# Optimization experiments

Measured on AMD Instinct MI355X. Metric: run time of the kernel, lower is better.

## Reference

```python
import jax, jax.numpy as jnp
import numpy as np

NUM_QUBITS = 10
NUM_LAYERS = 5
OBS = 10          # observation_size == num_qubits (required by input_scaling indexing)
NUM_OUTPUTS = 4   # num_actions, discretize=False
BATCH = 4096


def _bcast(theta, n):
    # theta: scalar or (B,) -> broadcastable against (B, 2, 2, ..., 2)
    return jnp.reshape(jnp.asarray(theta), (-1,) + (1,) * n)


def _ry(st, theta, q, n):
    # st: (B,) + (2,)*n complex64; per-sample RY(theta) on qubit q
    t = _bcast(theta, n) * 0.5
    c, s = jnp.cos(t), jnp.sin(t)
    s0 = jax.lax.index_in_dim(st, 0, axis=q + 1, keepdims=True)
    s1 = jax.lax.index_in_dim(st, 1, axis=q + 1, keepdims=True)
    return jnp.concatenate([c * s0 - s * s1, s * s0 + c * s1], axis=q + 1)


def _rz(st, theta, q, n):
    t = _bcast(theta, n) * 0.5
    s0 = jax.lax.index_in_dim(st, 0, axis=q + 1, keepdims=True)
    s1 = jax.lax.index_in_dim(st, 1, axis=q + 1, keepdims=True)
    return jnp.concatenate([jnp.exp(-1j * t) * s0, jnp.exp(1j * t) * s1], axis=q + 1)


def _cnot(st, c, t):
    # flip target axis on the control=1 slab; pure index ops (no residuals in bwd)
    s0 = jax.lax.index_in_dim(st, 0, axis=c + 1, keepdims=True)
    s1 = jax.lax.index_in_dim(st, 1, axis=c + 1, keepdims=True)
    s1 = jnp.flip(s1, axis=t + 1)
    return jnp.concatenate([s0, s1], axis=c + 1)


def _layer(st, x, isc, w, n, obs):
    # isc: (2n,) input_scaling row, w: (2n,) weights row
    for i in range(obs):
        st = _ry(st, isc[i] * x[:, i], i, n)
        st = _rz(st, isc[i + obs] * x[:, i], i, n)
    for i in range(n):
        st = _rz(st, w[i], i, n)
    for i in range(n):
        st = _ry(st, w[i + n], i, n)
    if n == 2:
        st = _cnot(st, 0, 1)
    else:
        for i in range(n):
            st = _cnot(st, i, (i + 1) % n)
    return st


_layer_ckpt = jax.checkpoint(_layer, static_argnums=(4, 5))


def _circuit(x, input_scaling, weights, n, num_layers, obs, num_outputs):
    B = x.shape[0]
    st = jnp.zeros((B,) + (2,) * n, dtype=jnp.complex64)
    st = st.at[(slice(None),) + (0,) * n].set(1.0)  # |0...0>
    for layer in range(num_layers):
        st = _layer_ckpt(st, x, input_scaling[layer], weights[layer], n, obs)
    probs = jnp.real(st * jnp.conj(st))
    outs = []
    for i in range(num_outputs):
        axes = tuple(a for a in range(1, n + 1) if a != i + 1)
        pi = jnp.sum(probs, axis=axes)  # (B, 2)
        outs.append(pi[:, 0] - pi[:, 1])  # <Z_i>
    return jnp.stack(outs, axis=1)


def setup_inputs() -> dict:
    key = jax.random.key(0)
    k1, k2 = jax.random.split(key)
    x = jax.random.normal(k1, (BATCH, OBS), dtype=jnp.float32)
    input_scaling = jnp.ones((NUM_LAYERS, 2 * NUM_QUBITS), dtype=jnp.float32)
    weights = jax.random.uniform(k2, (NUM_LAYERS, 2 * NUM_QUBITS), minval=-np.pi, maxval=np.pi, dtype=jnp.float32)
    output_scaling = jnp.ones((NUM_OUTPUTS,), dtype=jnp.float32)
    return {"x": x, "input_scaling": input_scaling, "weights": weights, "output_scaling": output_scaling}


def reference(x, input_scaling, weights, output_scaling):
    z = _circuit(x, input_scaling, weights, NUM_QUBITS, NUM_LAYERS, OBS, NUM_OUTPUTS)
    return z * output_scaling  # (B, num_actions); discretize=False -> actions = scaled expvals
```

## Files before the change

kernel.cpp:

```cpp
#include <hip/hip_runtime.h>


constexpr int NQ  = 10;
constexpr int NL  = 5;
constexpr int OBS = 10;

typedef float        f2 __attribute__((ext_vector_type(2)));
typedef _Float16     h2 __attribute__((ext_vector_type(2)));
typedef unsigned int u2 __attribute__((ext_vector_type(2)));
typedef int          i4 __attribute__((ext_vector_type(4)));

__device__ __forceinline__ float readlane_f(float v, int l) {
    return __int_as_float(__builtin_amdgcn_readlane(__float_as_int(v), l));
}
__device__ __forceinline__ int h2_to_i(h2 v) { int i; __builtin_memcpy(&i, &v, 4); return i; }
__device__ __forceinline__ h2  i_to_h2(int i) { h2 v; __builtin_memcpy(&v, &i, 4); return v; }

__device__ __forceinline__ h2 bperm_h2(int byte_addr, h2 v) {
    return i_to_h2(__builtin_amdgcn_ds_bpermute(byte_addr, h2_to_i(v)));
}
template <int CTRL>
__device__ __forceinline__ h2 dpp_h2(h2 v) {
    return i_to_h2(__builtin_amdgcn_update_dpp(0, h2_to_i(v), CTRL, 0xF, 0xF, true));
}
template <int M>
__device__ __forceinline__ h2 swz_h2(h2 v) {
    return i_to_h2(__builtin_amdgcn_ds_swizzle(h2_to_i(v), (M << 10) | 0x1F));
}

#if __has_builtin(__builtin_amdgcn_permlane16_swap) && __has_builtin(__builtin_amdgcn_permlane32_swap)
#define HAVE_PERMLANE_SWAP 1
#else
#define HAVE_PERMLANE_SWAP 0
#endif

__device__ __forceinline__ h2 xor_lane(h2 v, int M, int a16, int a32) {
    switch (M) {
    case 1:  return swz_h2<1>(v);
    case 2:  return swz_h2<2>(v);
    case 4:  return swz_h2<4>(v);
    case 8:  return swz_h2<8>(v);
    case 16: return bperm_h2(a16, v);
    default: return bperm_h2(a32, v);
    }
}

__device__ __forceinline__ float fold16_f(float z, int a16) {
#if HAVE_PERMLANE_SWAP
    u2 r = __builtin_amdgcn_permlane16_swap(
        __float_as_uint(z), __float_as_uint(z), false, false);
    return __uint_as_float(r[0]) + __uint_as_float(r[1]);
#else
    return z + __int_as_float(__builtin_amdgcn_ds_bpermute(a16, __float_as_int(z)));
#endif
}
__device__ __forceinline__ float fold32_f(float z, int a32) {
#if HAVE_PERMLANE_SWAP
    u2 r = __builtin_amdgcn_permlane32_swap(
        __float_as_uint(z), __float_as_uint(z), false, false);
    return __uint_as_float(r[0]) + __uint_as_float(r[1]);
#else
    return z + __int_as_float(__builtin_amdgcn_ds_bpermute(a32, __float_as_int(z)));
#endif
}

__device__ __forceinline__ h2 mk_h2(float a, float b) {
    h2 r; r.x = (_Float16)a; r.y = (_Float16)b; return r;
}
__device__ __forceinline__ h2 xor_h2(h2 v, int m) {
    return i_to_h2(h2_to_i(v) ^ m);
}

__global__ __launch_bounds__(256, 4) void qsim_kernel(
    const float* __restrict__ x,
    const float* __restrict__ isc,
    const float* __restrict__ w,
    const float* __restrict__ oscale,
    float* __restrict__ out,
    int B)
{
    const int lane  = threadIdx.x & 63;
    const int wslot = threadIdx.x >> 6;
    const int wid   = (blockIdx.x * blockDim.x + threadIdx.x) >> 6;
    if (wid >= B) return;

    __shared__ int ldsK[4][50 * 4];

    float cUR, cUI, cVR, cVI;
    {
        const int g   = (lane < 50) ? lane : 49;
        const int q   = g % 10;
        const int lyr = g / 10;
        const float xq    = x[wid * OBS + q];
        const float alpha = isc[lyr * 2 * NQ + q]      * xq;
        const float beta  = isc[lyr * 2 * NQ + NQ + q] * xq;
        const float gamma = w[lyr * 2 * NQ + q];
        const float delta = w[lyr * 2 * NQ + NQ + q];
        float sa, ca, sp, cp, sd, cd;
        __sincosf(0.5f * alpha,          &sa, &ca);
        __sincosf(0.5f * (beta + gamma), &sp, &cp);
        __sincosf(0.5f * delta,          &sd, &cd);
        const float A = cd * ca, Bt = sd * sa;
        const float C = cd * sa, D  = sd * ca;
        cUR = (A - Bt) * cp;
        cUI = -(A + Bt) * sp;
        cVR = (C + D) * cp;
        cVI = (C - D) * sp;
        if (lane < 50) {
            i4 pk;
            pk.x = h2_to_i(mk_h2(cUR,  cUR));
            pk.y = h2_to_i(mk_h2(-cUI, cUI));
            pk.z = h2_to_i(mk_h2(cVR,  cVR));
            pk.w = h2_to_i(mk_h2(-cVI, cVI));
            *reinterpret_cast<i4*>(&ldsK[wslot][lane * 4]) = pk;
        }
    }

    const int a16 = (lane ^ 16) * 4;
    const int a32 = (lane ^ 32) * 4;
    const int cnot_src  = (lane ^ (lane >> 1));
    const int addr_even = cnot_src * 4;
    const int addr_odd  = (cnot_src ^ 32) * 4;

    int smP[6];
#pragma unroll
    for (int qq = 0; qq < 6; ++qq) {
        const int M = 1 << (5 - qq);
        smP[qq] = (lane & M) ? (int)0x80008000 : 0;
    }

    h2 c[16];

    {
        float Lr = 1.f, Li = 0.f;
#pragma unroll
        for (int q = 4; q < 10; ++q) {
            const float ur = readlane_f(cUR, q), ui = readlane_f(cUI, q);
            const float vr = readlane_f(cVR, q), vi = readlane_f(cVI, q);
            const int M = 1 << (9 - q);
            const float fr = (lane & M) ? vr : ur;
            const float fi = (lane & M) ? vi : ui;
            const float nr = Lr * fr - Li * fi;
            const float ni = Lr * fi + Li * fr;
            Lr = nr; Li = ni;
        }
        f2 cf[16];
        cf[0] = (f2){Lr, Li};
#pragma unroll
        for (int r = 1; r < 16; ++r) cf[r] = (f2){0.f, 0.f};
#pragma unroll
        for (int q = 3; q >= 0; --q) {
            const int m = 1 << (3 - q);
            const float ur = readlane_f(cUR, q), ui = readlane_f(cUI, q);
            const float vr = readlane_f(cVR, q), vi = readlane_f(cVI, q);
#pragma unroll
            for (int r0 = 0; r0 < 16; ++r0) {
                if (r0 >= m) continue;
                const f2 s = cf[r0];
                cf[r0 | m] = (f2){ s.x*vr - s.y*vi, s.x*vi + s.y*vr };
                cf[r0]     = (f2){ s.x*ur - s.y*ui, s.x*ui + s.y*ur };
            }
        }
#pragma unroll
        for (int r = 0; r < 16; ++r) c[r] = mk_h2(cf[r].x, cf[r].y);
    }

#define SWAPR(i, j) { h2 _t = c[i]; c[i] = c[j]; c[j] = _t; }

    for (int layer = 0; layer < NL; ++layer) {
        const int base = layer * NQ;

        if (layer > 0) {
            h2 K[NQ][4];
#pragma unroll
            for (int q = 0; q < NQ; ++q) {
                const i4 pk = *reinterpret_cast<const i4*>(
                    &ldsK[wslot][(base + q) * 4]);
                K[q][0] = i_to_h2(pk.x);
                K[q][1] = i_to_h2(pk.y);
                K[q][2] = i_to_h2(pk.z);
                K[q][3] = i_to_h2(pk.w);
            }
#pragma unroll
            for (int q = 0; q < NQ; ++q) {
                const h2 kUU = K[q][0];
                const h2 kUI = K[q][1];
                const h2 kVV = K[q][2];
                const h2 kVI = K[q][3];

                if (q < 4) {
                    const int m = 1 << (3 - q);
#pragma unroll
                    for (int r0 = 0; r0 < 16; ++r0) {
                        if (r0 & m) continue;
                        const int r1 = r0 | m;
                        const h2 c0 = c[r0], c1 = c[r1];
                        const h2 c0s = c0.yx, c1s = c1.yx;
                        c[r0] = kUU*c0 + kUI*c0s - kVV*c1 + kVI*c1s;
                        c[r1] = kVV*c0 + kVI*c0s + kUU*c1 - kUI*c1s;
                    }
                } else {
                    const int  M  = 1 << (9 - q);
                    const int  sm = smP[q - 4];
                    const h2 kPI = xor_h2(kUI, sm);
                    const h2 kQR = xor_h2(-kVV, sm);
#pragma unroll
                    for (int r = 0; r < 16; ++r) {
                        const h2 mv = c[r];
                        const h2 pv = xor_lane(mv, M, a16, a32);
                        c[r] = kUU*mv + kPI*mv.yx + kQR*pv + kVI*pv.yx;
                    }
                }
            }
        }

        if (layer < NL - 1) {
            SWAPR(8, 12) SWAPR(9, 13) SWAPR(10, 14) SWAPR(11, 15)
            SWAPR(4, 6)  SWAPR(5, 7)  SWAPR(12, 14) SWAPR(13, 15)
            SWAPR(2, 3)  SWAPR(6, 7)  SWAPR(10, 11) SWAPR(14, 15)
#pragma unroll
            for (int r = 0; r < 16; ++r) {
                const int addr = (r & 1) ? addr_odd : addr_even;
                c[r] = bperm_h2(addr, c[r]);
            }
            const bool ctl = (lane & 1) != 0;
#pragma unroll
            for (int r = 0; r < 8; ++r) {
                const h2 t0 = c[r], t1 = c[r + 8];
                c[r]     = ctl ? t1 : t0;
                c[r + 8] = ctl ? t0 : t1;
            }
        }
    }

    f2 Z01 = (f2){0.f, 0.f}, Z23 = (f2){0.f, 0.f};
#pragma unroll
    for (int r = 0; r < 16; ++r) {
#if __has_builtin(__builtin_amdgcn_fdot2)
        const float pv = __builtin_amdgcn_fdot2(c[r], c[r], 0.0f, false);
#else
        const float cr = (float)c[r].x, ci = (float)c[r].y;
        const float pv = cr * cr + ci * ci;
#endif
        Z01 += (f2){ (__popc(r & 7)  & 1) ? -pv : pv,
                     (__popc(r & 12) & 1) ? -pv : pv };
        Z23 += (f2){ (__popc(r & 14) & 1) ? -pv : pv,
                     (__popc(r & 15) & 1) ? -pv : pv };
    }
    const float sL = (__popc(lane) & 1) ? -1.f : 1.f;
    float z0 = Z01.x * sL, z1 = Z01.y, z2 = Z23.x, z3 = Z23.y;
#pragma unroll
    for (int m = 1; m < 64; m <<= 1) {
        if (m == 1)      { z0 += __int_as_float(__builtin_amdgcn_update_dpp(0, __float_as_int(z0), 0xB1, 0xF, 0xF, true));
                           z1 += __int_as_float(__builtin_amdgcn_update_dpp(0, __float_as_int(z1), 0xB1, 0xF, 0xF, true));
                           z2 += __int_as_float(__builtin_amdgcn_update_dpp(0, __float_as_int(z2), 0xB1, 0xF, 0xF, true));
                           z3 += __int_as_float(__builtin_amdgcn_update_dpp(0, __float_as_int(z3), 0xB1, 0xF, 0xF, true)); }
        else if (m == 2) { z0 += __int_as_float(__builtin_amdgcn_update_dpp(0, __float_as_int(z0), 0x4E, 0xF, 0xF, true));
                           z1 += __int_as_float(__builtin_amdgcn_update_dpp(0, __float_as_int(z1), 0x4E, 0xF, 0xF, true));
                           z2 += __int_as_float(__builtin_amdgcn_update_dpp(0, __float_as_int(z2), 0x4E, 0xF, 0xF, true));
                           z3 += __int_as_float(__builtin_amdgcn_update_dpp(0, __float_as_int(z3), 0x4E, 0xF, 0xF, true)); }
        else if (m == 4) { z0 += __int_as_float(__builtin_amdgcn_update_dpp(0, __builtin_amdgcn_update_dpp(0, __float_as_int(z0), 0x1B, 0xF, 0xF, true), 0x141, 0xF, 0xF, true));
                           z1 += __int_as_float(__builtin_amdgcn_update_dpp(0, __builtin_amdgcn_update_dpp(0, __float_as_int(z1), 0x1B, 0xF, 0xF, true), 0x141, 0xF, 0xF, true));
                           z2 += __int_as_float(__builtin_amdgcn_update_dpp(0, __builtin_amdgcn_update_dpp(0, __float_as_int(z2), 0x1B, 0xF, 0xF, true), 0x141, 0xF, 0xF, true));
                           z3 += __int_as_float(__builtin_amdgcn_update_dpp(0, __builtin_amdgcn_update_dpp(0, __float_as_int(z3), 0x1B, 0xF, 0xF, true), 0x141, 0xF, 0xF, true)); }
        else if (m == 8) { z0 += __int_as_float(__builtin_amdgcn_update_dpp(0, __float_as_int(z0), 0x128, 0xF, 0xF, true));
                           z1 += __int_as_float(__builtin_amdgcn_update_dpp(0, __float_as_int(z1), 0x128, 0xF, 0xF, true));
                           z2 += __int_as_float(__builtin_amdgcn_update_dpp(0, __float_as_int(z2), 0x128, 0xF, 0xF, true));
                           z3 += __int_as_float(__builtin_amdgcn_update_dpp(0, __float_as_int(z3), 0x128, 0xF, 0xF, true)); }
        else if (m == 16){ z0 = fold16_f(z0, a16);
                           z1 = fold16_f(z1, a16);
                           z2 = fold16_f(z2, a16);
                           z3 = fold16_f(z3, a16); }
        else             { z0 = fold32_f(z0, a32);
                           z1 = fold32_f(z1, a32);
                           z2 = fold32_f(z2, a32);
                           z3 = fold32_f(z3, a32); }
    }
    if (lane == 0) {
        out[wid * 4 + 0] = z0 * oscale[0];
        out[wid * 4 + 1] = z1 * oscale[1];
        out[wid * 4 + 2] = z2 * oscale[2];
        out[wid * 4 + 3] = z3 * oscale[3];
    }
#undef SWAPR
}

extern "C" void kernel_launch(void* const* d_in, const int* in_sizes, int n_in,
                              void* d_out, int out_size, void* d_ws, size_t ws_size,
                              hipStream_t stream) {
    const float* x      = (const float*)d_in[0];
    const float* isc    = (const float*)d_in[1];
    const float* w      = (const float*)d_in[2];
    const float* oscale = (const float*)d_in[3];
    float* out = (float*)d_out;

    const int B = in_sizes[0] / OBS;
    const int threads = 256;
    const int blocks = (B * 64 + threads - 1) / threads;
    qsim_kernel<<<blocks, threads, 0, stream>>>(x, isc, w, oscale, out, B);
}
```

Before: 84.68 us.

## Reorder CNOT select before lane permute and prefetch next layer coefficients

The CNOT ring now does the control-conditioned register select before the cross-lane bpermute, using a precomputed parity predicate, and loads the next layer's LDS coefficients between them so the LDS latency overlaps the permutes. The xor-16 lane exchange switches from bpermute to ds_swizzle. The initial state build uses packed f2 complex multiplies, and the f16 conversion uses cvt_pkrtz. These target LDS and permute latency and the conversion instruction count, in exchange for more live registers from the hoisted coefficient array and round-toward-zero instead of round-to-nearest f16 conversion.

```diff
diff --git a/kernel.cpp b/kernel.cpp
--- a/kernel.cpp
+++ b/kernel.cpp
@@ -19,10 +19,6 @@
 __device__ __forceinline__ h2 bperm_h2(int byte_addr, h2 v) {
     return i_to_h2(__builtin_amdgcn_ds_bpermute(byte_addr, h2_to_i(v)));
 }
-template <int CTRL>
-__device__ __forceinline__ h2 dpp_h2(h2 v) {
-    return i_to_h2(__builtin_amdgcn_update_dpp(0, h2_to_i(v), CTRL, 0xF, 0xF, true));
-}
 template <int M>
 __device__ __forceinline__ h2 swz_h2(h2 v) {
     return i_to_h2(__builtin_amdgcn_ds_swizzle(h2_to_i(v), (M << 10) | 0x1F));
@@ -34,13 +30,13 @@
 #define HAVE_PERMLANE_SWAP 0
 #endif
 
-__device__ __forceinline__ h2 xor_lane(h2 v, int M, int a16, int a32) {
+__device__ __forceinline__ h2 xor_lane(h2 v, int M, int a32) {
     switch (M) {
     case 1:  return swz_h2<1>(v);
     case 2:  return swz_h2<2>(v);
     case 4:  return swz_h2<4>(v);
     case 8:  return swz_h2<8>(v);
-    case 16: return bperm_h2(a16, v);
+    case 16: return swz_h2<16>(v);
     default: return bperm_h2(a32, v);
     }
 }
@@ -66,6 +62,14 @@
 
 __device__ __forceinline__ h2 mk_h2(float a, float b) {
     h2 r; r.x = (_Float16)a; r.y = (_Float16)b; return r;
+}
+__device__ __forceinline__ h2 pk_h2(float a, float b) {
+#if __has_builtin(__builtin_amdgcn_cvt_pkrtz)
+    auto t = __builtin_amdgcn_cvt_pkrtz(a, b);
+    h2 r; __builtin_memcpy(&r, &t, 4); return r;
+#else
+    return mk_h2(a, b);
+#endif
 }
 __device__ __forceinline__ h2 xor_h2(h2 v, int m) {
     return i_to_h2(h2_to_i(v) ^ m);
@@ -121,6 +125,8 @@
     const int cnot_src  = (lane ^ (lane >> 1));
     const int addr_even = cnot_src * 4;
     const int addr_odd  = (cnot_src ^ 32) * 4;
+    const bool ctlE = (__popc(lane) & 1) != 0;
+    const bool ctlO = !ctlE;
 
     int smP[6];
 #pragma unroll
@@ -130,22 +136,34 @@
     }
 
     h2 c[16];
+    h2 Kc[NQ][4];
+
+    auto loadK = [&](int lyr) {
+#pragma unroll
+        for (int q = 0; q < NQ; ++q) {
+            const i4 pk = *reinterpret_cast<const i4*>(
+                &ldsK[wslot][(lyr * NQ + q) * 4]);
+            Kc[q][0] = i_to_h2(pk.x);
+            Kc[q][1] = i_to_h2(pk.y);
+            Kc[q][2] = i_to_h2(pk.z);
+            Kc[q][3] = i_to_h2(pk.w);
+        }
+    };
 
     {
-        float Lr = 1.f, Li = 0.f;
+        f2 L = (f2){1.f, 0.f};
 #pragma unroll
         for (int q = 4; q < 10; ++q) {
             const float ur = readlane_f(cUR, q), ui = readlane_f(cUI, q);
             const float vr = readlane_f(cVR, q), vi = readlane_f(cVI, q);
             const int M = 1 << (9 - q);
-            const float fr = (lane & M) ? vr : ur;
-            const float fi = (lane & M) ? vi : ui;
-            const float nr = Lr * fr - Li * fi;
-            const float ni = Lr * fi + Li * fr;
-            Lr = nr; Li = ni;
+            const bool b = (lane & M) != 0;
+            const f2 F1 = (f2){ b ? vr : ur,  b ? vi : ui };
+            const f2 F2 = (f2){ -F1.y, F1.x };
+            L = (f2){L.x, L.x} * F1 + (f2){L.y, L.y} * F2;
         }
         f2 cf[16];
-        cf[0] = (f2){Lr, Li};
+        cf[0] = L;
 #pragma unroll
         for (int r = 1; r < 16; ++r) cf[r] = (f2){0.f, 0.f};
 #pragma unroll
@@ -153,84 +171,79 @@
             const int m = 1 << (3 - q);
             const float ur = readlane_f(cUR, q), ui = readlane_f(cUI, q);
             const float vr = readlane_f(cVR, q), vi = readlane_f(cVI, q);
+            const f2 U1 = (f2){ur, ui}, U2 = (f2){-ui, ur};
+            const f2 V1 = (f2){vr, vi}, V2 = (f2){-vi, vr};
 #pragma unroll
             for (int r0 = 0; r0 < 16; ++r0) {
                 if (r0 >= m) continue;
-                const f2 s = cf[r0];
-                cf[r0 | m] = (f2){ s.x*vr - s.y*vi, s.x*vi + s.y*vr };
-                cf[r0]     = (f2){ s.x*ur - s.y*ui, s.x*ui + s.y*ur };
+                const f2 s  = cf[r0];
+                const f2 sx = (f2){s.x, s.x}, sy = (f2){s.y, s.y};
+                cf[r0 | m] = sx * V1 + sy * V2;
+                cf[r0]     = sx * U1 + sy * U2;
             }
         }
 #pragma unroll
-        for (int r = 0; r < 16; ++r) c[r] = mk_h2(cf[r].x, cf[r].y);
+        for (int r = 0; r < 16; ++r) c[r] = pk_h2(cf[r].x, cf[r].y);
     }
 
 #define SWAPR(i, j) { h2 _t = c[i]; c[i] = c[j]; c[j] = _t; }
-
-    for (int layer = 0; layer < NL; ++layer) {
-        const int base = layer * NQ;
-
-        if (layer > 0) {
-            h2 K[NQ][4];
-#pragma unroll
-            for (int q = 0; q < NQ; ++q) {
-                const i4 pk = *reinterpret_cast<const i4*>(
-                    &ldsK[wslot][(base + q) * 4]);
-                K[q][0] = i_to_h2(pk.x);
-                K[q][1] = i_to_h2(pk.y);
-                K[q][2] = i_to_h2(pk.z);
-                K[q][3] = i_to_h2(pk.w);
-            }
-#pragma unroll
-            for (int q = 0; q < NQ; ++q) {
-                const h2 kUU = K[q][0];
-                const h2 kUI = K[q][1];
-                const h2 kVV = K[q][2];
-                const h2 kVI = K[q][3];
-
-                if (q < 4) {
-                    const int m = 1 << (3 - q);
-#pragma unroll
-                    for (int r0 = 0; r0 < 16; ++r0) {
-                        if (r0 & m) continue;
-                        const int r1 = r0 | m;
-                        const h2 c0 = c[r0], c1 = c[r1];
-                        const h2 c0s = c0.yx, c1s = c1.yx;
-                        c[r0] = kUU*c0 + kUI*c0s - kVV*c1 + kVI*c1s;
-                        c[r1] = kVV*c0 + kVI*c0s + kUU*c1 - kUI*c1s;
-                    }
-                } else {
-                    const int  M  = 1 << (9 - q);
-                    const int  sm = smP[q - 4];
-                    const h2 kPI = xor_h2(kUI, sm);
-                    const h2 kQR = xor_h2(-kVV, sm);
-#pragma unroll
-                    for (int r = 0; r < 16; ++r) {
-                        const h2 mv = c[r];
-                        const h2 pv = xor_lane(mv, M, a16, a32);
-                        c[r] = kUU*mv + kPI*mv.yx + kQR*pv + kVI*pv.yx;
-                    }
+#define RING(nextL)                                                     \
+    {                                                                   \
+        SWAPR(8, 12) SWAPR(9, 13) SWAPR(10, 14) SWAPR(11, 15)           \
+        SWAPR(4, 6)  SWAPR(5, 7)  SWAPR(12, 14) SWAPR(13, 15)           \
+        SWAPR(2, 3)  SWAPR(6, 7)  SWAPR(10, 11) SWAPR(14, 15)           \
+        _Pragma("unroll")                                               \
+        for (int r = 0; r < 8; ++r) {                                   \
+            const bool ct = (r & 1) ? ctlO : ctlE;                      \
+            const h2 t0 = c[r], t1 = c[r + 8];                          \
+            c[r]     = ct ? t1 : t0;                                    \
+            c[r + 8] = ct ? t0 : t1;                                    \
+        }                                                               \
+        loadK(nextL);                                                   \
+        _Pragma("unroll")                                               \
+        for (int r = 0; r < 16; ++r) {                                  \
+            const int addr = (r & 1) ? addr_odd : addr_even;            \
+            c[r] = bperm_h2(addr, c[r]);                                \
+        }                                                               \
+    }
+
+    RING(1)
+
+    for (int layer = 1; layer < NL; ++layer) {
+#pragma unroll
+        for (int q = 0; q < NQ; ++q) {
+            const h2 kUU = Kc[q][0];
+            const h2 kUI = Kc[q][1];
+            const h2 kVV = Kc[q][2];
+            const h2 kVI = Kc[q][3];
+
+            if (q < 4) {
+                const int m = 1 << (3 - q);
+#pragma unroll
+                for (int r0 = 0; r0 < 16; ++r0) {
+                    if (r0 & m) continue;
+                    const int r1 = r0 | m;
+                    const h2 c0 = c[r0], c1 = c[r1];
+                    const h2 c0s = c0.yx, c1s = c1.yx;
+                    c[r0] = kUU*c0 + kUI*c0s - kVV*c1 + kVI*c1s;
+                    c[r1] = kVV*c0 + kVI*c0s + kUU*c1 - kUI*c1s;
+                }
+            } else {
+                const int  M  = 1 << (9 - q);
+                const int  sm = smP[q - 4];
+                const h2 kPI = xor_h2(kUI, sm);
+                const h2 kQR = xor_h2(-kVV, sm);
+#pragma unroll
+                for (int r = 0; r < 16; ++r) {
+                    const h2 mv = c[r];
+                    const h2 pv = xor_lane(mv, M, a32);
+                    c[r] = kUU*mv + kPI*mv.yx + kQR*pv + kVI*pv.yx;
                 }
             }
         }
-
-        if (layer < NL - 1) {
-            SWAPR(8, 12) SWAPR(9, 13) SWAPR(10, 14) SWAPR(11, 15)
-            SWAPR(4, 6)  SWAPR(5, 7)  SWAPR(12, 14) SWAPR(13, 15)
-            SWAPR(2, 3)  SWAPR(6, 7)  SWAPR(10, 11) SWAPR(14, 15)
-#pragma unroll
-            for (int r = 0; r < 16; ++r) {
-                const int addr = (r & 1) ? addr_odd : addr_even;
-                c[r] = bperm_h2(addr, c[r]);
-            }
-            const bool ctl = (lane & 1) != 0;
-#pragma unroll
-            for (int r = 0; r < 8; ++r) {
-                const h2 t0 = c[r], t1 = c[r + 8];
-                c[r]     = ctl ? t1 : t0;
-                c[r + 8] = ctl ? t0 : t1;
-            }
-        }
+        if (layer == 1) { RING(2) }
+        else if (layer == 2) { RING(3) }
+        else if (layer == 3) { RING(4) }
     }
 
     f2 Z01 = (f2){0.f, 0.f}, Z23 = (f2){0.f, 0.f};
@@ -247,7 +260,7 @@
         Z23 += (f2){ (__popc(r & 14) & 1) ? -pv : pv,
                      (__popc(r & 15) & 1) ? -pv : pv };
     }
-    const float sL = (__popc(lane) & 1) ? -1.f : 1.f;
+    const float sL = ctlE ? -1.f : 1.f;
     float z0 = Z01.x * sL, z1 = Z01.y, z2 = Z23.x, z3 = Z23.y;
 #pragma unroll
     for (int m = 1; m < 64; m <<= 1) {
@@ -282,6 +295,7 @@
         out[wid * 4 + 2] = z2 * oscale[2];
         out[wid * 4 + 3] = z3 * oscale[3];
     }
+#undef RING
 #undef SWAPR
 }
 
```

Result: no change. 83.86 us (-1.0%).
